# Performance work log

Measured on AMD Instinct MI355X. Metric: run time of the kernel, lower is better.

Reference implementation:

```python
import jax, jax.numpy as jnp
import numpy as np

N_NODES = 50000
N_EDGES = 800000
D_IN = 128
D_OUT = 128  # hidden_size == output_size == 128


def setup_inputs() -> dict:
    key = jax.random.key(0)
    k_x, k_src, k_dst, k_w1, k_w2 = jax.random.split(key, 5)
    x = jax.random.normal(k_x, (N_NODES, D_IN), dtype=jnp.float32)
    src = jax.random.randint(k_src, (N_EDGES,), 0, N_NODES)
    dst = jax.random.randint(k_dst, (N_EDGES,), 0, N_NODES)
    # SGConv fc weight (torch Linear layout: [out, in]) and bias
    w_conv = jax.random.normal(k_w1, (D_OUT, D_IN), dtype=jnp.float32) / np.sqrt(D_IN)
    b_conv = jnp.zeros((D_OUT,), dtype=jnp.float32)
    # trailing Linear(hidden_size=128 -> output_size=128)
    w_lin = jax.random.normal(k_w2, (D_OUT, D_OUT), dtype=jnp.float32) / np.sqrt(D_OUT)
    b_lin = jnp.zeros((D_OUT,), dtype=jnp.float32)
    return {"x": x, "src": src, "dst": dst,
            "w_conv": w_conv, "b_conv": b_conv,
            "w_lin": w_lin, "b_lin": b_lin}


def reference(x, src, dst, w_conv, b_conv, w_lin, b_lin):
    n = x.shape[0]
    # symmetric normalization by in-degree (DGL SGConv, k=1 hop)
    deg = jax.ops.segment_sum(jnp.ones_like(dst, dtype=x.dtype), dst, num_segments=n)
    norm = jax.lax.rsqrt(jnp.clip(deg, 1.0))[:, None]  # [N,1]
    h = x * norm                                        # D^{-1/2} X
    h = jax.ops.segment_sum(h[src], dst, num_segments=n)  # A (D^{-1/2} X), spmm via gather+scatter-add
    h = h * norm                                        # D^{-1/2} A D^{-1/2} X
    h = jnp.maximum(h @ w_conv.T + b_conv, 0.0)         # SGConv fc + relu
    return jnp.maximum(h @ w_lin.T + b_lin, 0.0)        # Linear + relu
```

## Files before the change

kernel.cpp:

```cpp
#include <hip/hip_runtime.h>


#define D 128
#define SCAN_TILE 1024

typedef __attribute__((ext_vector_type(8))) short short8;
typedef __attribute__((ext_vector_type(4))) float f32x4;

__device__ __forceinline__ unsigned short f2bf(float f) {
    union { float f; unsigned u; } c; c.f = f;
    unsigned u = c.u;
    unsigned r = u + 0x7FFFu + ((u >> 16) & 1u);
    return (unsigned short)(r >> 16);
}
__device__ __forceinline__ float bf2f(unsigned short b) {
    union { unsigned u; float f; } c; c.u = ((unsigned)b) << 16;
    return c.f;
}

__global__ __launch_bounds__(256) void degree_kernel(const int* __restrict__ dst,
                                                     int* __restrict__ deg, int E) {
    int e = blockIdx.x * blockDim.x + threadIdx.x;
    if (e < E) atomicAdd(&deg[dst[e]], 1);
}

__global__ __launch_bounds__(256) void scan_partial_kernel(const int* __restrict__ deg,
                                                           int* __restrict__ blockSums, int N) {
    int tid = threadIdx.x;
    int base = blockIdx.x * SCAN_TILE + (tid << 2);
    int4 v = make_int4(0, 0, 0, 0);
    if (base + 3 < N) v = *(const int4*)(deg + base);
    else {
        if (base + 0 < N) v.x = deg[base + 0];
        if (base + 1 < N) v.y = deg[base + 1];
        if (base + 2 < N) v.z = deg[base + 2];
        if (base + 3 < N) v.w = deg[base + 3];
    }
    int s = v.x + v.y + v.z + v.w;
    for (int off = 32; off; off >>= 1) s += __shfl_down(s, off, 64);
    __shared__ int ws[4];
    if ((tid & 63) == 0) ws[tid >> 6] = s;
    __syncthreads();
    if (tid == 0) blockSums[blockIdx.x] = ws[0] + ws[1] + ws[2] + ws[3];
}

__global__ __launch_bounds__(256) void scan_blocksums_kernel(int* __restrict__ blockSums, int B) {
    __shared__ int s[256];
    int tid = threadIdx.x;
    int v = (tid < B) ? blockSums[tid] : 0;
    s[tid] = v;
    __syncthreads();
    for (int off = 1; off < 256; off <<= 1) {
        int u = (tid >= off) ? s[tid - off] : 0;
        __syncthreads();
        s[tid] += u;
        __syncthreads();
    }
    if (tid < B) blockSums[tid] = (tid == 0) ? 0 : s[tid - 1];
}

__global__ __launch_bounds__(256) void scan_final_kernel(
    const int* __restrict__ deg, const int* __restrict__ blockSums,
    int* __restrict__ row_start, int* __restrict__ cursor,
    float* __restrict__ norm, int N, int E) {
    int tid = threadIdx.x;
    int base = blockIdx.x * SCAN_TILE + (tid << 2);
    int4 v = make_int4(0, 0, 0, 0);
    if (base + 3 < N) v = *(const int4*)(deg + base);
    else {
        if (base + 0 < N) v.x = deg[base + 0];
        if (base + 1 < N) v.y = deg[base + 1];
        if (base + 2 < N) v.z = deg[base + 2];
        if (base + 3 < N) v.w = deg[base + 3];
    }
    int local = v.x + v.y + v.z + v.w;
    int lane = tid & 63, w = tid >> 6;
    int inc = local;
    for (int off = 1; off < 64; off <<= 1) {
        int u = __shfl_up(inc, off, 64);
        if (lane >= off) inc += u;
    }
    __shared__ int wsum[4];
    if (lane == 63) wsum[w] = inc;
    __syncthreads();
    int woff = 0;
    for (int i = 0; i < w; ++i) woff += wsum[i];
    int ex = (inc - local) + woff + blockSums[blockIdx.x];
    int4 rs;
    rs.x = ex;
    rs.y = rs.x + v.x;
    rs.z = rs.y + v.y;
    rs.w = rs.z + v.z;
    float4 nm;
    nm.x = rsqrtf(fmaxf((float)v.x, 1.0f));
    nm.y = rsqrtf(fmaxf((float)v.y, 1.0f));
    nm.z = rsqrtf(fmaxf((float)v.z, 1.0f));
    nm.w = rsqrtf(fmaxf((float)v.w, 1.0f));
    if (base + 3 < N) {
        *(int4*)(row_start + base) = rs;
        *(int4*)(cursor + base) = rs;
        *(float4*)(norm + base) = nm;
    } else {
        if (base + 0 < N) { row_start[base + 0] = rs.x; cursor[base + 0] = rs.x; norm[base + 0] = nm.x; }
        if (base + 1 < N) { row_start[base + 1] = rs.y; cursor[base + 1] = rs.y; norm[base + 1] = nm.y; }
        if (base + 2 < N) { row_start[base + 2] = rs.z; cursor[base + 2] = rs.z; norm[base + 2] = nm.z; }
    }
    if (blockIdx.x == 0 && tid == 0) row_start[N] = E;
}

__global__ __launch_bounds__(256) void binning_kernel(
    const int* __restrict__ src, const int* __restrict__ dst,
    int* __restrict__ cursor, unsigned short* __restrict__ sorted16, int E) {
    int e = blockIdx.x * blockDim.x + threadIdx.x;
    if (e < E) {
        int d = dst[e];
        int s = src[e];
        int p = atomicAdd(&cursor[d], 1);
        sorted16[p] = (unsigned short)s;
    }
}

__global__ void scale_kernel(const float* __restrict__ x, const float* __restrict__ norm,
                             unsigned short* __restrict__ xsb, int N) {
    int idx = blockIdx.x * blockDim.x + threadIdx.x;
    int total = N * (D / 4);
    if (idx >= total) return;
    int row = idx >> 5;
    float nrm = norm[row];
    float4 v = ((const float4*)x)[idx];
    ushort4 o;
    o.x = f2bf(v.x * nrm);
    o.y = f2bf(v.y * nrm);
    o.z = f2bf(v.z * nrm);
    o.w = f2bf(v.w * nrm);
    ((ushort4*)xsb)[idx] = o;
}

__device__ __forceinline__ void addbf4(float4& a, ushort4 u) {
    a.x += bf2f(u.x);
    a.y += bf2f(u.y);
    a.z += bf2f(u.z);
    a.w += bf2f(u.w);
}

__global__ __launch_bounds__(256) void aggregate_kernel(
    const unsigned short* __restrict__ xsb, const unsigned short* __restrict__ sorted16,
    const int* __restrict__ row_start, const float* __restrict__ norm,
    unsigned short* __restrict__ h2hi, unsigned short* __restrict__ h2lo, int N) {
    int wave = (int)((blockIdx.x * blockDim.x + threadIdx.x) >> 6);
    int lane = threadIdx.x & 63;
    if (wave >= N) return;
    int s = row_start[wave];
    int t = row_start[wave + 1];
    int c4 = (lane & 31) << 2;
    int half = lane >> 5;
    float4 acc = make_float4(0.f, 0.f, 0.f, 0.f);
    for (int base = s; base < t; base += 64) {
        int cnt = min(64, t - base);
        int my = (lane < cnt) ? (int)sorted16[base + lane] : 0;
        int j = 0;
        for (; j + 15 < cnt; j += 16) {
            int i0 = __shfl(my, j + 0 + half, 64);
            int i1 = __shfl(my, j + 2 + half, 64);
            int i2 = __shfl(my, j + 4 + half, 64);
            int i3 = __shfl(my, j + 6 + half, 64);
            int i4 = __shfl(my, j + 8 + half, 64);
            int i5 = __shfl(my, j + 10 + half, 64);
            int i6 = __shfl(my, j + 12 + half, 64);
            int i7 = __shfl(my, j + 14 + half, 64);
            ushort4 u0 = *(const ushort4*)(xsb + (size_t)i0 * D + c4);
            ushort4 u1 = *(const ushort4*)(xsb + (size_t)i1 * D + c4);
            ushort4 u2 = *(const ushort4*)(xsb + (size_t)i2 * D + c4);
            ushort4 u3 = *(const ushort4*)(xsb + (size_t)i3 * D + c4);
            ushort4 u4 = *(const ushort4*)(xsb + (size_t)i4 * D + c4);
            ushort4 u5 = *(const ushort4*)(xsb + (size_t)i5 * D + c4);
            ushort4 u6 = *(const ushort4*)(xsb + (size_t)i6 * D + c4);
            ushort4 u7 = *(const ushort4*)(xsb + (size_t)i7 * D + c4);
            addbf4(acc, u0); addbf4(acc, u1); addbf4(acc, u2); addbf4(acc, u3);
            addbf4(acc, u4); addbf4(acc, u5); addbf4(acc, u6); addbf4(acc, u7);
        }
        for (; j + 1 < cnt; j += 2) {
            int i0 = __shfl(my, j + half, 64);
            ushort4 u0 = *(const ushort4*)(xsb + (size_t)i0 * D + c4);
            addbf4(acc, u0);
        }
        if (j < cnt) {
            int i0 = __shfl(my, j, 64);
            if (half == 0) {
                ushort4 u0 = *(const ushort4*)(xsb + (size_t)i0 * D + c4);
                addbf4(acc, u0);
            }
        }
    }
    acc.x += __shfl_xor(acc.x, 32, 64);
    acc.y += __shfl_xor(acc.y, 32, 64);
    acc.z += __shfl_xor(acc.z, 32, 64);
    acc.w += __shfl_xor(acc.w, 32, 64);
    if (half == 0) {
        float nrm = norm[wave];
        float o[4] = {acc.x * nrm, acc.y * nrm, acc.z * nrm, acc.w * nrm};
        ushort4 hv, lv;
        unsigned short* hp = (unsigned short*)&hv;
        unsigned short* lp = (unsigned short*)&lv;
        #pragma unroll
        for (int q = 0; q < 4; ++q) {
            unsigned short h = f2bf(o[q]);
            float r = o[q] - bf2f(h);
            hp[q] = h;
            lp[q] = f2bf(r);
        }
        *(ushort4*)(h2hi + (size_t)wave * D + c4) = hv;
        *(ushort4*)(h2lo + (size_t)wave * D + c4) = lv;
    }
}

__global__ __launch_bounds__(256) void prep_w_kernel(
    const float* __restrict__ wc, const float* __restrict__ wl,
    unsigned short* __restrict__ w1c, unsigned short* __restrict__ w2c,
    unsigned short* __restrict__ w1l, unsigned short* __restrict__ w2l) {
    int idx = blockIdx.x * 256 + threadIdx.x;
    const float* src = (idx < 16384) ? wc : wl;
    int j = idx & 16383;
    float x = src[j];
    unsigned short c1 = f2bf(x);
    float r = x - bf2f(c1);
    unsigned short c2 = f2bf(r);
    if (idx < 16384) { w1c[j] = c1; w2c[j] = c2; }
    else             { w1l[j] = c1; w2l[j] = c2; }
}

__device__ __forceinline__ void layer_bf(
    const unsigned short* shi, const unsigned short* slo,
    const unsigned short* __restrict__ w1, const unsigned short* __restrict__ w2,
    const float* __restrict__ bias,
    f32x4 acc[2][4], int wr0, int wc0, int lm, int lg) {
    #pragma unroll
    for (int mt = 0; mt < 2; ++mt)
        #pragma unroll
        for (int nt = 0; nt < 4; ++nt) {
            float b = bias[wc0 + nt * 16 + lm];
            acc[mt][nt] = (f32x4){b, b, b, b};
        }
    #pragma unroll
    for (int k0 = 0; k0 < 128; k0 += 32) {
        short8 ahi[2], alo[2];
        #pragma unroll
        for (int mt = 0; mt < 2; ++mt) {
            int row = wr0 + mt * 16 + lm;
            int slot = (k0 >> 3) + lg;
            int off = row * 128 + (((slot) ^ (row & 7)) << 3);
            ahi[mt] = *(const short8*)(shi + off);
            alo[mt] = *(const short8*)(slo + off);
        }
        #pragma unroll
        for (int nt = 0; nt < 4; ++nt) {
            int widx = (wc0 + nt * 16 + lm) * 128 + k0 + lg * 8;
            short8 bhi = *(const short8*)(w1 + widx);
            short8 blo = *(const short8*)(w2 + widx);
            #pragma unroll
            for (int mt = 0; mt < 2; ++mt) {
                f32x4 c = acc[mt][nt];
                c = __builtin_amdgcn_mfma_f32_16x16x32_bf16(ahi[mt], blo, c, 0, 0, 0);
                c = __builtin_amdgcn_mfma_f32_16x16x32_bf16(alo[mt], bhi, c, 0, 0, 0);
                c = __builtin_amdgcn_mfma_f32_16x16x32_bf16(ahi[mt], bhi, c, 0, 0, 0);
                acc[mt][nt] = c;
            }
        }
    }
}

__device__ __forceinline__ void store_bf(
    unsigned short* shi, unsigned short* slo,
    f32x4 acc[2][4], int wr0, int wc0, int lm, int lg) {
    #pragma unroll
    for (int mt = 0; mt < 2; ++mt)
        #pragma unroll
        for (int nt = 0; nt < 4; ++nt)
            #pragma unroll
            for (int j = 0; j < 4; ++j) {
                int row = wr0 + mt * 16 + lg * 4 + j;
                int col = wc0 + nt * 16 + lm;
                float v = fmaxf(acc[mt][nt][j], 0.0f);
                unsigned short h = f2bf(v);
                float r = v - bf2f(h);
                int off = row * 128 + (((col >> 3) ^ (row & 7)) << 3) + (col & 7);
                shi[off] = h;
                slo[off] = f2bf(r);
            }
}

__global__ __launch_bounds__(256, 2) void mlp_mfma_kernel(
    const unsigned short* __restrict__ h2hi, const unsigned short* __restrict__ h2lo,
    const unsigned short* __restrict__ w1c, const unsigned short* __restrict__ w2c,
    const float* __restrict__ bc,
    const unsigned short* __restrict__ w1l, const unsigned short* __restrict__ w2l,
    const float* __restrict__ bl,
    float* __restrict__ out, int N) {
    __shared__ unsigned short shi[64 * 128];
    __shared__ unsigned short slo[64 * 128];
    int tid = threadIdx.x;
    int row0 = blockIdx.x * 64;

    #pragma unroll
    for (int i = 0; i < 4; ++i) {
        int f = i * 256 + tid;
        int r = f >> 4, sl = f & 15;
        int grow = row0 + r;
        short8 vh = (short8){0,0,0,0,0,0,0,0};
        short8 vl = (short8){0,0,0,0,0,0,0,0};
        if (grow < N) {
            vh = *(const short8*)(h2hi + (size_t)grow * D + sl * 8);
            vl = *(const short8*)(h2lo + (size_t)grow * D + sl * 8);
        }
        int off = r * 128 + ((sl ^ (r & 7)) << 3);
        *(short8*)(shi + off) = vh;
        *(short8*)(slo + off) = vl;
    }
    __syncthreads();

    int w = tid >> 6, lane = tid & 63;
    int lm = lane & 15, lg = lane >> 4;
    int wr0 = (w >> 1) * 32, wc0 = (w & 1) * 64;

    f32x4 acc[2][4];

    layer_bf(shi, slo, w1c, w2c, bc, acc, wr0, wc0, lm, lg);
    __syncthreads();
    store_bf(shi, slo, acc, wr0, wc0, lm, lg);
    __syncthreads();

    layer_bf(shi, slo, w1l, w2l, bl, acc, wr0, wc0, lm, lg);

    #pragma unroll
    for (int mt = 0; mt < 2; ++mt)
        #pragma unroll
        for (int j = 0; j < 4; ++j) {
            int row = row0 + wr0 + mt * 16 + lg * 4 + j;
            if (row < N) {
                #pragma unroll
                for (int nt = 0; nt < 4; ++nt)
                    out[(size_t)row * D + wc0 + nt * 16 + lm] = fmaxf(acc[mt][nt][j], 0.0f);
            }
        }
}

extern "C" void kernel_launch(void* const* d_in, const int* in_sizes, int n_in,
                              void* d_out, int out_size, void* d_ws, size_t ws_size,
                              hipStream_t stream) {
    const float* x      = (const float*)d_in[0];
    const int*   src    = (const int*)d_in[1];
    const int*   dst    = (const int*)d_in[2];
    const float* wc     = (const float*)d_in[3];
    const float* bc     = (const float*)d_in[4];
    const float* wl     = (const float*)d_in[5];
    const float* bl     = (const float*)d_in[6];
    float* out = (float*)d_out;

    int N = in_sizes[0] / D;
    int E = in_sizes[1];

    size_t off = 0;
    auto carve = [&](size_t bytes) -> void* {
        void* p = (char*)d_ws + off;
        off += (bytes + 255) & ~(size_t)255;
        return p;
    };
    unsigned short* xsb       = (unsigned short*)carve((size_t)N * D * 2);
    unsigned short* h2hi      = (unsigned short*)carve((size_t)N * D * 2);
    unsigned short* h2lo      = (unsigned short*)carve((size_t)N * D * 2);
    int*            deg       = (int*)carve((size_t)N * 4);
    int*            row_start = (int*)carve((size_t)(N + 1) * 4);
    int*            cursor    = (int*)carve((size_t)N * 4);
    float*          norm      = (float*)carve((size_t)N * 4);
    int*            blockSums = (int*)carve(1024 * 4);
    unsigned short* sorted16  = (unsigned short*)carve((size_t)E * 2);
    unsigned short* w1c = (unsigned short*)carve(16384 * 2);
    unsigned short* w2c = (unsigned short*)carve(16384 * 2);
    unsigned short* w1l = (unsigned short*)carve(16384 * 2);
    unsigned short* w2l = (unsigned short*)carve(16384 * 2);
    (void)ws_size;

    hipMemsetAsync(deg, 0, (size_t)N * 4, stream);

    int nScanBlocks = (N + SCAN_TILE - 1) / SCAN_TILE;

    prep_w_kernel<<<128, 256, 0, stream>>>(wc, wl, w1c, w2c, w1l, w2l);
    degree_kernel<<<(E + 255) / 256, 256, 0, stream>>>(dst, deg, E);
    scan_partial_kernel<<<nScanBlocks, 256, 0, stream>>>(deg, blockSums, N);
    scan_blocksums_kernel<<<1, 256, 0, stream>>>(blockSums, nScanBlocks);
    scan_final_kernel<<<nScanBlocks, 256, 0, stream>>>(deg, blockSums, row_start, cursor, norm, N, E);
    binning_kernel<<<(E + 255) / 256, 256, 0, stream>>>(src, dst, cursor, sorted16, E);
    {
        int total = N * (D / 4);
        scale_kernel<<<(total + 255) / 256, 256, 0, stream>>>(x, norm, xsb, N);
    }
    aggregate_kernel<<<(N + 3) / 4, 256, 0, stream>>>(xsb, sorted16, row_start, norm, h2hi, h2lo, N);
    mlp_mfma_kernel<<<(N + 63) / 64, 256, 0, stream>>>(h2hi, h2lo, w1c, w2c, bc, w1l, w2l, bl, out, N);
}
```

Baseline: 244.2 us.

## Privatize degree and binning counters into per-block-group partitions

Splits the degree histogram and the binning cursors into 8 copies selected by block index, so atomics on the same destination node from different blocks hit separate addresses. Two new kernels sum the partitions into the degree array and set up per-partition cursor offsets from row_start. This aims to reduce atomic contention and serialization in the degree and binning passes. In exchange it adds two kernel launches, a larger memset and extra memory traffic for the 8x counter arrays. The int4 loads in the new kernels assume N is a multiple of 4.

```diff
diff --git a/kernel.cpp b/kernel.cpp
--- a/kernel.cpp
+++ b/kernel.cpp
@@ -3,6 +3,7 @@
 
 #define D 128
 #define SCAN_TILE 1024
+#define NPART 8
 
 typedef __attribute__((ext_vector_type(8))) short short8;
 typedef __attribute__((ext_vector_type(4))) float f32x4;
@@ -19,9 +20,22 @@
 }
 
 __global__ __launch_bounds__(256) void degree_kernel(const int* __restrict__ dst,
-                                                     int* __restrict__ deg, int E) {
+                                                     int* __restrict__ deg8, int N, int E) {
     int e = blockIdx.x * blockDim.x + threadIdx.x;
-    if (e < E) atomicAdd(&deg[dst[e]], 1);
+    if (e < E) atomicAdd(&deg8[(blockIdx.x & (NPART - 1)) * N + dst[e]], 1);
+}
+
+__global__ __launch_bounds__(256) void reduce_deg_kernel(const int* __restrict__ deg8,
+                                                         int* __restrict__ deg, int N) {
+    int base = (blockIdx.x * blockDim.x + threadIdx.x) << 2;
+    if (base >= N) return;
+    int4 s = make_int4(0, 0, 0, 0);
+    #pragma unroll
+    for (int x = 0; x < NPART; ++x) {
+        int4 v = *(const int4*)(deg8 + (size_t)x * N + base);
+        s.x += v.x; s.y += v.y; s.z += v.z; s.w += v.w;
+    }
+    *(int4*)(deg + base) = s;
 }
 
 __global__ __launch_bounds__(256) void scan_partial_kernel(const int* __restrict__ deg,
@@ -61,8 +75,7 @@
 
 __global__ __launch_bounds__(256) void scan_final_kernel(
     const int* __restrict__ deg, const int* __restrict__ blockSums,
-    int* __restrict__ row_start, int* __restrict__ cursor,
-    float* __restrict__ norm, int N, int E) {
+    int* __restrict__ row_start, float* __restrict__ norm, int N, int E) {
     int tid = threadIdx.x;
     int base = blockIdx.x * SCAN_TILE + (tid << 2);
     int4 v = make_int4(0, 0, 0, 0);
@@ -98,24 +111,37 @@
     nm.w = rsqrtf(fmaxf((float)v.w, 1.0f));
     if (base + 3 < N) {
         *(int4*)(row_start + base) = rs;
-        *(int4*)(cursor + base) = rs;
         *(float4*)(norm + base) = nm;
     } else {
-        if (base + 0 < N) { row_start[base + 0] = rs.x; cursor[base + 0] = rs.x; norm[base + 0] = nm.x; }
-        if (base + 1 < N) { row_start[base + 1] = rs.y; cursor[base + 1] = rs.y; norm[base + 1] = nm.y; }
-        if (base + 2 < N) { row_start[base + 2] = rs.z; cursor[base + 2] = rs.z; norm[base + 2] = nm.z; }
+        if (base + 0 < N) { row_start[base + 0] = rs.x; norm[base + 0] = nm.x; }
+        if (base + 1 < N) { row_start[base + 1] = rs.y; norm[base + 1] = nm.y; }
+        if (base + 2 < N) { row_start[base + 2] = rs.z; norm[base + 2] = nm.z; }
     }
     if (blockIdx.x == 0 && tid == 0) row_start[N] = E;
+}
+
+__global__ __launch_bounds__(256) void cursor_init_kernel(
+    const int* __restrict__ deg8, const int* __restrict__ row_start,
+    int* __restrict__ curX, int N) {
+    int base = (blockIdx.x * blockDim.x + threadIdx.x) << 2;
+    if (base >= N) return;
+    int4 run = *(const int4*)(row_start + base);
+    #pragma unroll
+    for (int x = 0; x < NPART; ++x) {
+        *(int4*)(curX + (size_t)x * N + base) = run;
+        int4 v = *(const int4*)(deg8 + (size_t)x * N + base);
+        run.x += v.x; run.y += v.y; run.z += v.z; run.w += v.w;
+    }
 }
 
 __global__ __launch_bounds__(256) void binning_kernel(
     const int* __restrict__ src, const int* __restrict__ dst,
-    int* __restrict__ cursor, unsigned short* __restrict__ sorted16, int E) {
+    int* __restrict__ curX, unsigned short* __restrict__ sorted16, int N, int E) {
     int e = blockIdx.x * blockDim.x + threadIdx.x;
     if (e < E) {
         int d = dst[e];
         int s = src[e];
-        int p = atomicAdd(&cursor[d], 1);
+        int p = atomicAdd(&curX[(blockIdx.x & (NPART - 1)) * N + d], 1);
         sorted16[p] = (unsigned short)s;
     }
 }
@@ -368,9 +394,10 @@
     unsigned short* xsb       = (unsigned short*)carve((size_t)N * D * 2);
     unsigned short* h2hi      = (unsigned short*)carve((size_t)N * D * 2);
     unsigned short* h2lo      = (unsigned short*)carve((size_t)N * D * 2);
+    int*            deg8      = (int*)carve((size_t)NPART * N * 4);
     int*            deg       = (int*)carve((size_t)N * 4);
     int*            row_start = (int*)carve((size_t)(N + 1) * 4);
-    int*            cursor    = (int*)carve((size_t)N * 4);
+    int*            curX      = (int*)carve((size_t)NPART * N * 4);
     float*          norm      = (float*)carve((size_t)N * 4);
     int*            blockSums = (int*)carve(1024 * 4);
     unsigned short* sorted16  = (unsigned short*)carve((size_t)E * 2);
@@ -380,16 +407,18 @@
     unsigned short* w2l = (unsigned short*)carve(16384 * 2);
     (void)ws_size;
 
-    hipMemsetAsync(deg, 0, (size_t)N * 4, stream);
+    hipMemsetAsync(deg8, 0, (size_t)NPART * N * 4, stream);
 
     int nScanBlocks = (N + SCAN_TILE - 1) / SCAN_TILE;
 
     prep_w_kernel<<<128, 256, 0, stream>>>(wc, wl, w1c, w2c, w1l, w2l);
-    degree_kernel<<<(E + 255) / 256, 256, 0, stream>>>(dst, deg, E);
+    degree_kernel<<<(E + 255) / 256, 256, 0, stream>>>(dst, deg8, N, E);
+    reduce_deg_kernel<<<(N / 4 + 255) / 256, 256, 0, stream>>>(deg8, deg, N);
     scan_partial_kernel<<<nScanBlocks, 256, 0, stream>>>(deg, blockSums, N);
     scan_blocksums_kernel<<<1, 256, 0, stream>>>(blockSums, nScanBlocks);
-    scan_final_kernel<<<nScanBlocks, 256, 0, stream>>>(deg, blockSums, row_start, cursor, norm, N, E);
-    binning_kernel<<<(E + 255) / 256, 256, 0, stream>>>(src, dst, cursor, sorted16, E);
+    scan_final_kernel<<<nScanBlocks, 256, 0, stream>>>(deg, blockSums, row_start, norm, N, E);
+    cursor_init_kernel<<<(N / 4 + 255) / 256, 256, 0, stream>>>(deg8, row_start, curX, N);
+    binning_kernel<<<(E + 255) / 256, 256, 0, stream>>>(src, dst, curX, sorted16, N, E);
     {
         int total = N * (D / 4);
         scale_kernel<<<(total + 255) / 256, 256, 0, stream>>>(x, norm, xsb, N);
```

Result: no change. 244.5 us (+0.1%).

## Record per-edge rank during degree count and pad degree counters

Applied to the files above, without the earlier changes.

The degree-count kernel now keeps the value returned by its atomicAdd as a per-edge rank, so CSR binning becomes a plain scatter (row_start[dst] + rank) instead of a second pass of atomics on a cursor array. Degree counters are padded to one per 64 bytes to cut contention between neighbouring nodes' atomics. The trade-off is a 16x larger counter array to memset and read with strided loads during the scan, plus an extra E-sized rank buffer.

```diff
diff --git a/kernel.cpp b/kernel.cpp
--- a/kernel.cpp
+++ b/kernel.cpp
@@ -3,6 +3,7 @@
 
 #define D 128
 #define SCAN_TILE 1024
+#define PAD 16
 
 typedef __attribute__((ext_vector_type(8))) short short8;
 typedef __attribute__((ext_vector_type(4))) float f32x4;
@@ -18,24 +19,25 @@
     return c.f;
 }
 
-__global__ __launch_bounds__(256) void degree_kernel(const int* __restrict__ dst,
-                                                     int* __restrict__ deg, int E) {
+__global__ __launch_bounds__(256) void degree_rank_kernel(
+    const int* __restrict__ dst, int* __restrict__ degp,
+    unsigned short* __restrict__ rank16, int E) {
     int e = blockIdx.x * blockDim.x + threadIdx.x;
-    if (e < E) atomicAdd(&deg[dst[e]], 1);
-}
-
-__global__ __launch_bounds__(256) void scan_partial_kernel(const int* __restrict__ deg,
+    if (e < E) {
+        int p = atomicAdd(&degp[dst[e] * PAD], 1);
+        rank16[e] = (unsigned short)p;
+    }
+}
+
+__global__ __launch_bounds__(256) void scan_partial_kernel(const int* __restrict__ degp,
                                                            int* __restrict__ blockSums, int N) {
     int tid = threadIdx.x;
     int base = blockIdx.x * SCAN_TILE + (tid << 2);
     int4 v = make_int4(0, 0, 0, 0);
-    if (base + 3 < N) v = *(const int4*)(deg + base);
-    else {
-        if (base + 0 < N) v.x = deg[base + 0];
-        if (base + 1 < N) v.y = deg[base + 1];
-        if (base + 2 < N) v.z = deg[base + 2];
-        if (base + 3 < N) v.w = deg[base + 3];
-    }
+    if (base + 0 < N) v.x = degp[(base + 0) * PAD];
+    if (base + 1 < N) v.y = degp[(base + 1) * PAD];
+    if (base + 2 < N) v.z = degp[(base + 2) * PAD];
+    if (base + 3 < N) v.w = degp[(base + 3) * PAD];
     int s = v.x + v.y + v.z + v.w;
     for (int off = 32; off; off >>= 1) s += __shfl_down(s, off, 64);
     __shared__ int ws[4];
@@ -60,19 +62,15 @@
 }
 
 __global__ __launch_bounds__(256) void scan_final_kernel(
-    const int* __restrict__ deg, const int* __restrict__ blockSums,
-    int* __restrict__ row_start, int* __restrict__ cursor,
-    float* __restrict__ norm, int N, int E) {
+    const int* __restrict__ degp, const int* __restrict__ blockSums,
+    int* __restrict__ row_start, float* __restrict__ norm, int N, int E) {
     int tid = threadIdx.x;
     int base = blockIdx.x * SCAN_TILE + (tid << 2);
     int4 v = make_int4(0, 0, 0, 0);
-    if (base + 3 < N) v = *(const int4*)(deg + base);
-    else {
-        if (base + 0 < N) v.x = deg[base + 0];
-        if (base + 1 < N) v.y = deg[base + 1];
-        if (base + 2 < N) v.z = deg[base + 2];
-        if (base + 3 < N) v.w = deg[base + 3];
-    }
+    if (base + 0 < N) v.x = degp[(base + 0) * PAD];
+    if (base + 1 < N) v.y = degp[(base + 1) * PAD];
+    if (base + 2 < N) v.z = degp[(base + 2) * PAD];
+    if (base + 3 < N) v.w = degp[(base + 3) * PAD];
     int local = v.x + v.y + v.z + v.w;
     int lane = tid & 63, w = tid >> 6;
     int inc = local;
@@ -98,25 +96,24 @@
     nm.w = rsqrtf(fmaxf((float)v.w, 1.0f));
     if (base + 3 < N) {
         *(int4*)(row_start + base) = rs;
-        *(int4*)(cursor + base) = rs;
         *(float4*)(norm + base) = nm;
     } else {
-        if (base + 0 < N) { row_start[base + 0] = rs.x; cursor[base + 0] = rs.x; norm[base + 0] = nm.x; }
-        if (base + 1 < N) { row_start[base + 1] = rs.y; cursor[base + 1] = rs.y; norm[base + 1] = nm.y; }
-        if (base + 2 < N) { row_start[base + 2] = rs.z; cursor[base + 2] = rs.z; norm[base + 2] = nm.z; }
+        if (base + 0 < N) { row_start[base + 0] = rs.x; norm[base + 0] = nm.x; }
+        if (base + 1 < N) { row_start[base + 1] = rs.y; norm[base + 1] = nm.y; }
+        if (base + 2 < N) { row_start[base + 2] = rs.z; norm[base + 2] = nm.z; }
     }
     if (blockIdx.x == 0 && tid == 0) row_start[N] = E;
 }
 
-__global__ __launch_bounds__(256) void binning_kernel(
+__global__ __launch_bounds__(256) void scatter_kernel(
     const int* __restrict__ src, const int* __restrict__ dst,
-    int* __restrict__ cursor, unsigned short* __restrict__ sorted16, int E) {
+    const unsigned short* __restrict__ rank16, const int* __restrict__ row_start,
+    unsigned short* __restrict__ sorted16, int E) {
     int e = blockIdx.x * blockDim.x + threadIdx.x;
     if (e < E) {
         int d = dst[e];
-        int s = src[e];
-        int p = atomicAdd(&cursor[d], 1);
-        sorted16[p] = (unsigned short)s;
+        int p = row_start[d] + (int)rank16[e];
+        sorted16[p] = (unsigned short)src[e];
     }
 }
 
@@ -368,11 +365,11 @@
     unsigned short* xsb       = (unsigned short*)carve((size_t)N * D * 2);
     unsigned short* h2hi      = (unsigned short*)carve((size_t)N * D * 2);
     unsigned short* h2lo      = (unsigned short*)carve((size_t)N * D * 2);
-    int*            deg       = (int*)carve((size_t)N * 4);
+    int*            degp      = (int*)carve((size_t)N * PAD * 4);
     int*            row_start = (int*)carve((size_t)(N + 1) * 4);
-    int*            cursor    = (int*)carve((size_t)N * 4);
     float*          norm      = (float*)carve((size_t)N * 4);
     int*            blockSums = (int*)carve(1024 * 4);
+    unsigned short* rank16    = (unsigned short*)carve((size_t)E * 2);
     unsigned short* sorted16  = (unsigned short*)carve((size_t)E * 2);
     unsigned short* w1c = (unsigned short*)carve(16384 * 2);
     unsigned short* w2c = (unsigned short*)carve(16384 * 2);
@@ -380,16 +377,16 @@
     unsigned short* w2l = (unsigned short*)carve(16384 * 2);
     (void)ws_size;
 
-    hipMemsetAsync(deg, 0, (size_t)N * 4, stream);
+    hipMemsetAsync(degp, 0, (size_t)N * PAD * 4, stream);
 
     int nScanBlocks = (N + SCAN_TILE - 1) / SCAN_TILE;
 
     prep_w_kernel<<<128, 256, 0, stream>>>(wc, wl, w1c, w2c, w1l, w2l);
-    degree_kernel<<<(E + 255) / 256, 256, 0, stream>>>(dst, deg, E);
-    scan_partial_kernel<<<nScanBlocks, 256, 0, stream>>>(deg, blockSums, N);
+    degree_rank_kernel<<<(E + 255) / 256, 256, 0, stream>>>(dst, degp, rank16, E);
+    scan_partial_kernel<<<nScanBlocks, 256, 0, stream>>>(degp, blockSums, N);
     scan_blocksums_kernel<<<1, 256, 0, stream>>>(blockSums, nScanBlocks);
-    scan_final_kernel<<<nScanBlocks, 256, 0, stream>>>(deg, blockSums, row_start, cursor, norm, N, E);
-    binning_kernel<<<(E + 255) / 256, 256, 0, stream>>>(src, dst, cursor, sorted16, E);
+    scan_final_kernel<<<nScanBlocks, 256, 0, stream>>>(degp, blockSums, row_start, norm, N, E);
+    scatter_kernel<<<(E + 255) / 256, 256, 0, stream>>>(src, dst, rank16, row_start, sorted16, E);
     {
         int total = N * (D / 4);
         scale_kernel<<<(total + 255) / 256, 256, 0, stream>>>(x, norm, xsb, N);
```

New measurement: 213.6 us. 12.5% less time.
